# Kernel tuning notes

Measured on AMD Instinct MI355X. Metric: run time of the kernel, lower is better.

Reference implementation:

```python
import jax, jax.numpy as jnp
import numpy as np

QMIN_A, QMAX_A = -128, 127  # int8 activation range
GROUPSIZE = 32


def per_token_quant_dequant(x):
    """Dynamic per-token asymmetric int8 fake-quant (torchao per_token_dynamic_quant)."""
    min_val = jnp.minimum(jnp.min(x, axis=-1, keepdims=True), 0.0)
    max_val = jnp.maximum(jnp.max(x, axis=-1, keepdims=True), 0.0)
    scale = (max_val - min_val) / float(QMAX_A - QMIN_A)
    scale = jnp.maximum(scale, jnp.finfo(x.dtype).eps)
    zp = jnp.clip(QMIN_A - jnp.round(min_val / scale), QMIN_A, QMAX_A)
    q = jnp.clip(jnp.round(x / scale) + zp, QMIN_A, QMAX_A)
    return (q - zp) * scale


def dequant_int4_grouped(w_int, w_scales, w_zeros):
    """w_int: [O, I] int4 values in [-8, 7]; scales/zeros: [O, I//GROUPSIZE]."""
    O, I = w_int.shape
    G = I // GROUPSIZE
    wg = w_int.reshape(O, G, GROUPSIZE).astype(w_scales.dtype)
    w_dq = (wg - w_zeros[:, :, None]) * w_scales[:, :, None]
    return w_dq.reshape(O, I)


def setup_inputs() -> dict:
    key = jax.random.key(0)
    k1, k2, k3 = jax.random.split(key, 3)
    B, S, D_IN, D_OUT = 4, 2048, 2048, 2048
    G = D_IN // GROUPSIZE
    x = jax.random.normal(k1, (B, S, D_IN), dtype=jnp.float32)
    w_int = jax.random.randint(k2, (D_OUT, D_IN), -8, 8, dtype=jnp.int32)
    w_scales = jax.random.uniform(k3, (D_OUT, G), dtype=jnp.float32) * 0.01 + 1e-3
    w_zeros = jnp.zeros((D_OUT, G), dtype=jnp.float32)
    return {"x": x, "w_int": w_int, "w_scales": w_scales, "w_zeros": w_zeros}


def reference(x, w_int, w_scales, w_zeros):
    x_dq = per_token_quant_dequant(x)                  # [B, S, I]
    w_dq = dequant_int4_grouped(w_int, w_scales, w_zeros)  # [O, I]
    return jnp.einsum("bsi,oi->bso", x_dq, w_dq)       # [B, S, O]
```

## Files before the change

kernel.cpp:

```cpp
#include <hip/hip_runtime.h>

#define M_DIM 8192
#define N_DIM 2048
#define K_DIM 2048

#define BM 256
#define BN 256
#define BK 64
#define NT (K_DIM / BK)

#define AS1 __attribute__((address_space(1)))
#define AS3 __attribute__((address_space(3)))

typedef float f32x4 __attribute__((ext_vector_type(4)));
typedef short s16x8 __attribute__((ext_vector_type(8)));

__device__ __forceinline__ unsigned short f2bf(float f) {
  unsigned int u = __float_as_uint(f);
  u += 0x7FFFu + ((u >> 16) & 1u);
  return (unsigned short)(u >> 16);
}

__global__ __launch_bounds__(256) void prep_kernel(
    const float* __restrict__ x, const int* __restrict__ w,
    const float* __restrict__ ws, const float* __restrict__ wz,
    unsigned short* __restrict__ A, unsigned short* __restrict__ W) {
  const int tid = threadIdx.x;
  if (blockIdx.x < M_DIM) {
    const int t = blockIdx.x;
    const float4* r4 = (const float4*)(x + (size_t)t * K_DIM);
    float4 v0 = r4[tid];
    float4 v1 = r4[tid + 256];

    float mn = fminf(fminf(fminf(v0.x, v0.y), fminf(v0.z, v0.w)),
                     fminf(fminf(v1.x, v1.y), fminf(v1.z, v1.w)));
    float mx = fmaxf(fmaxf(fmaxf(v0.x, v0.y), fmaxf(v0.z, v0.w)),
                     fmaxf(fmaxf(v1.x, v1.y), fmaxf(v1.z, v1.w)));
#pragma unroll
    for (int off = 32; off > 0; off >>= 1) {
      mn = fminf(mn, __shfl_xor(mn, off));
      mx = fmaxf(mx, __shfl_xor(mx, off));
    }
    __shared__ float smn[4], smx[4];
    if ((tid & 63) == 0) { smn[tid >> 6] = mn; smx[tid >> 6] = mx; }
    __syncthreads();
    mn = fminf(fminf(smn[0], smn[1]), fminf(smn[2], smn[3]));
    mx = fmaxf(fmaxf(smx[0], smx[1]), fmaxf(smx[2], smx[3]));
    mn = fminf(mn, 0.0f);
    mx = fmaxf(mx, 0.0f);

    float scale = (mx - mn) / 255.0f;
    scale = fmaxf(scale, 1.1920928955078125e-07f);
    const float inv = 1.0f / scale;
    float zp = -128.0f - rintf(mn * inv);
    zp = fminf(fmaxf(zp, -128.0f), 127.0f);

    ushort4* Ao = (ushort4*)(A + (size_t)t * K_DIM);
    {
      float q; ushort4 r;
      q = rintf(v0.x * inv) + zp; q = fminf(fmaxf(q, -128.f), 127.f); r.x = f2bf((q - zp) * scale);
      q = rintf(v0.y * inv) + zp; q = fminf(fmaxf(q, -128.f), 127.f); r.y = f2bf((q - zp) * scale);
      q = rintf(v0.z * inv) + zp; q = fminf(fmaxf(q, -128.f), 127.f); r.z = f2bf((q - zp) * scale);
      q = rintf(v0.w * inv) + zp; q = fminf(fmaxf(q, -128.f), 127.f); r.w = f2bf((q - zp) * scale);
      Ao[tid] = r;
    }
    {
      float q; ushort4 r;
      q = rintf(v1.x * inv) + zp; q = fminf(fmaxf(q, -128.f), 127.f); r.x = f2bf((q - zp) * scale);
      q = rintf(v1.y * inv) + zp; q = fminf(fmaxf(q, -128.f), 127.f); r.y = f2bf((q - zp) * scale);
      q = rintf(v1.z * inv) + zp; q = fminf(fmaxf(q, -128.f), 127.f); r.z = f2bf((q - zp) * scale);
      q = rintf(v1.w * inv) + zp; q = fminf(fmaxf(q, -128.f), 127.f); r.w = f2bf((q - zp) * scale);
      Ao[tid + 256] = r;
    }
  } else {
    const int idx = (blockIdx.x - M_DIM) * 256 + tid;
    const int o  = idx >> 8;
    const int ii = (idx & 255) * 8;
    const int g  = ii >> 5;
    const float s = ws[o * 64 + g];
    const float z = wz[o * 64 + g];
    const int4* wp = (const int4*)(w + (size_t)o * K_DIM + ii);
    int4 a = wp[0], b = wp[1];
    ushort4 r0, r1;
    r0.x = f2bf(((float)a.x - z) * s);
    r0.y = f2bf(((float)a.y - z) * s);
    r0.z = f2bf(((float)a.z - z) * s);
    r0.w = f2bf(((float)a.w - z) * s);
    r1.x = f2bf(((float)b.x - z) * s);
    r1.y = f2bf(((float)b.y - z) * s);
    r1.z = f2bf(((float)b.z - z) * s);
    r1.w = f2bf(((float)b.w - z) * s);
    ushort4* Wo = (ushort4*)(W + (size_t)o * K_DIM + ii);
    Wo[0] = r0;
    Wo[1] = r1;
  }
}


#define SFENCE() __builtin_amdgcn_sched_barrier(0)

#define DSR(dst, addr, IMM)                                                  \
  asm volatile("ds_read_b128 %0, %1 offset:%2"                               \
               : "=v"(dst) : "v"(addr), "i"(IMM))

#define LGKM_GATE(N)                                                         \
  do {                                                                       \
    asm volatile("s_waitcnt lgkmcnt(%0)" :: "i"(N) : "memory");              \
    SFENCE();                                                                \
  } while (0)

#define RD_A(dst, MH, PLIT)                                                  \
  do {                                                                       \
    _Pragma("unroll") for (int i = 0; i < 4; ++i) {                          \
      _Pragma("unroll") for (int kk = 0; kk < 2; ++kk) {                     \
        DSR(dst[i][kk], a_addr[kk],                                          \
            (PLIT) * 32768 + ((MH) * 4 + i) * 2048);                         \
      }                                                                      \
    }                                                                        \
  } while (0)

#define RD_B(dst, NH, PLIT)                                                  \
  do {                                                                       \
    _Pragma("unroll") for (int j = 0; j < 2; ++j) {                          \
      _Pragma("unroll") for (int kk = 0; kk < 2; ++kk) {                     \
        DSR(dst[j][kk], b_addr[kk],                                          \
            (PLIT) * 32768 + ((NH) * 2 + j) * 2048);                         \
      }                                                                      \
    }                                                                        \
  } while (0)

#define MFMA_Q(afX, bfX, MH, NH)                                             \
  do {                                                                       \
    __builtin_amdgcn_s_setprio(1);                                           \
    _Pragma("unroll") for (int kk = 0; kk < 2; ++kk) {                       \
      _Pragma("unroll") for (int i = 0; i < 4; ++i) {                        \
        _Pragma("unroll") for (int j = 0; j < 2; ++j) {                      \
          acc[(MH) * 4 + i][(NH) * 2 + j] =                                  \
              __builtin_amdgcn_mfma_f32_16x16x32_bf16(                       \
                  afX[i][kk], bfX[j][kk],                                    \
                  acc[(MH) * 4 + i][(NH) * 2 + j], 0, 0, 0);                 \
        }                                                                    \
      }                                                                      \
    }                                                                        \
    __builtin_amdgcn_s_setprio(0);                                           \
  } while (0)

#define STAGE_A_HALF(KN, DSTP, H)                                            \
  do {                                                                       \
    _Pragma("unroll") for (int j = 0; j < 2; ++j) {                          \
      __builtin_amdgcn_global_load_lds(                                      \
          (const AS1 void*)(ag + (size_t)((H) * 2 + j) * 64 * K_DIM + (KN)), \
          (AS3 void*)(&As[(DSTP) * (BM * BK) + ((H) * 2 + j) * 4096 + tid * 8]), \
          16, 0, 0);                                                         \
    }                                                                        \
  } while (0)

#define STAGE_B_HALF(KN, DSTP, H)                                            \
  do {                                                                       \
    _Pragma("unroll") for (int j = 0; j < 2; ++j) {                          \
      __builtin_amdgcn_global_load_lds(                                      \
          (const AS1 void*)(bg + (size_t)((H) * 2 + j) * 64 * K_DIM + (KN)), \
          (AS3 void*)(&Bs[(DSTP) * (BN * BK) + ((H) * 2 + j) * 4096 + tid * 8]), \
          16, 0, 0);                                                         \
    }                                                                        \
  } while (0)

#define ITER(KT, PLIT, BN0, BN1)                                             \
  {                                                                          \
    const int k1 = ((KT) + 1) * BK;                                          \
    const int k2 = ((KT) + 2) * BK;                                          \
       \
    RD_B(BN1, 1, PLIT);                                                      \
    RD_A(af1, 1, PLIT);                                                      \
    if ((KT) + 1 < NT) {                                                     \
      STAGE_A_HALF(k1, (PLIT) ^ 1, 1);                                       \
      STAGE_B_HALF(k1, (PLIT) ^ 1, 0);                                       \
      STAGE_B_HALF(k1, (PLIT) ^ 1, 1);                                       \
    }                                                                        \
    SFENCE();                                                                \
    LGKM_GATE(12);                \
    MFMA_Q(af0, BN0, 0, 0);                                                  \
    SFENCE();                                                                \
    LGKM_GATE(8);                                             \
    MFMA_Q(af0, BN1, 0, 1);                                                  \
    SFENCE();                                                                \
    LGKM_GATE(0);                      \
    MFMA_Q(af1, BN1, 1, 1);                                                  \
    SFENCE();                                                                \
    __builtin_amdgcn_s_barrier();             \
    SFENCE();                                                                \
                                                         \
    if ((KT) + 2 < NT) STAGE_A_HALF(k2, PLIT, 0);                            \
    SFENCE();                                                                \
    if ((KT) + 2 < NT) {                                                     \
      asm volatile("s_waitcnt vmcnt(2)" ::: "memory");                       \
    } else {                                                                 \
      asm volatile("s_waitcnt vmcnt(0)" ::: "memory");                       \
    }                                                                        \
    SFENCE();                                                                \
    __builtin_amdgcn_s_barrier();            \
    SFENCE();                                                                \
          \
    if ((KT) + 1 < NT) {                                                     \
      RD_A(af0, 0, (PLIT) ^ 1);                                              \
      RD_B(BN1, 0, (PLIT) ^ 1);          \
    }                                                                        \
    SFENCE();                                                                \
    MFMA_Q(af1, BN0, 1, 0);              \
  }

__global__ __launch_bounds__(512, 2) void gemm_kernel(
    const unsigned short* __restrict__ A,
    const unsigned short* __restrict__ B,
    float* __restrict__ C) {
  __shared__ unsigned short As[2 * BM * BK];
  __shared__ unsigned short Bs[2 * BN * BK];

  const int tid = threadIdx.x;
  const int id  = blockIdx.y * 8 + blockIdx.x;
  const int nid = (id & 7) * 32 + (id >> 3);
  const int bm  = (nid >> 3) * BM;
  const int bn  = (nid & 7) * BN;

  const int lane  = tid & 63;
  const int wv    = tid >> 6;
  const int waveM = (wv >> 2) * 128;
  const int waveN = (wv & 3) * 64;
  const int quad  = lane >> 4;
  const int l16   = lane & 15;

  const int trow = tid >> 3;
  const int phys = (tid & 7) ^ (trow & 7);
  const unsigned short* ag = A + (size_t)(bm + trow) * K_DIM + phys * 8;
  const unsigned short* bg = B + (size_t)(bn + trow) * K_DIM + phys * 8;

  const unsigned asb = (unsigned)(size_t)(AS3 void*)&As[0];
  const unsigned bsb = (unsigned)(size_t)(AS3 void*)&Bs[0];
  unsigned a_addr[2], b_addr[2];
#pragma unroll
  for (int kk = 0; kk < 2; ++kk) {
    const unsigned sw = (unsigned)((quad ^ (l16 & 7) ^ (kk * 4)) * 16);
    a_addr[kk] = asb + (unsigned)((waveM + l16) * BK * 2) + sw;
    b_addr[kk] = bsb + (unsigned)((waveN + l16) * BK * 2) + sw;
  }

  f32x4 acc[8][4] = {};
  s16x8 af0[4][2], af1[4][2];
  s16x8 bX[2][2], bY[2][2];

  STAGE_A_HALF(0, 0, 0);
  STAGE_A_HALF(0, 0, 1);
  STAGE_B_HALF(0, 0, 0);
  STAGE_B_HALF(0, 0, 1);
  STAGE_A_HALF(BK, 1, 0);
  SFENCE();
  asm volatile("s_waitcnt vmcnt(2)" ::: "memory");
  SFENCE();
  __builtin_amdgcn_s_barrier();
  SFENCE();
  RD_A(af0, 0, 0);
  RD_B(bX, 0, 0);
  SFENCE();

  for (int kt = 0; kt < NT; kt += 2) {
    ITER(kt, 0, bX, bY);
    ITER(kt + 1, 1, bY, bX);
  }

#pragma unroll
  for (int mi = 0; mi < 8; ++mi) {
#pragma unroll
    for (int ni = 0; ni < 4; ++ni) {
      const int o = bn + waveN + ni * 16 + l16;
#pragma unroll
      for (int r = 0; r < 4; ++r) {
        const int row = bm + waveM + mi * 16 + quad * 4 + r;
        C[(size_t)row * N_DIM + o] = acc[mi][ni][r];
      }
    }
  }
}

extern "C" void kernel_launch(void* const* d_in, const int* in_sizes, int n_in,
                              void* d_out, int out_size, void* d_ws, size_t ws_size,
                              hipStream_t stream) {
  const float* x        = (const float*)d_in[0];
  const int*   w_int    = (const int*)d_in[1];
  const float* w_scales = (const float*)d_in[2];
  const float* w_zeros  = (const float*)d_in[3];
  float* out = (float*)d_out;

  unsigned short* Aq = (unsigned short*)d_ws;
  unsigned short* Wq = Aq + (size_t)M_DIM * K_DIM;

  const int prep_blocks = M_DIM + (N_DIM * (K_DIM / 8)) / 256;
  prep_kernel<<<prep_blocks, 256, 0, stream>>>(x, w_int, w_scales, w_zeros, Aq, Wq);
  dim3 grid(N_DIM / BN, M_DIM / BM);
  gemm_kernel<<<grid, 512, 0, stream>>>(Aq, Wq, out);
}
```

Baseline: 182.3 us.

## Restructure GEMM main loop into barrier-separated phases with staggered A/B prefetch

Reorganizes each K-iteration of the bf16 MFMA GEMM into four barrier-delimited phases. Each phase reads a fragment from LDS, issues one half-tile global-to-LDS load (A for the next tile, B two tiles ahead), then runs one quadrant of MFMAs. The prologue now preloads B for the first two tiles, and the vmcnt waits are adjusted to match. The aim is to spread LDS reads and global loads evenly across the MFMA work and shorten register lifetimes. The cost is extra workgroup barriers per iteration, which can stall waves.

```diff
diff --git a/kernel.cpp b/kernel.cpp
--- a/kernel.cpp
+++ b/kernel.cpp
@@ -165,48 +165,52 @@
     }                                                                        \
   } while (0)
 
-#define ITER(KT, PLIT, BN0, BN1)                                             \
+#define PHASE_BAR()                                                          \
+  do {                                                                       \
+    SFENCE();                                                                \
+    __builtin_amdgcn_s_barrier();                                            \
+    SFENCE();                                                                \
+  } while (0)
+
+#define ITER(KT, PLIT)                                                       \
   {                                                                          \
     const int k1 = ((KT) + 1) * BK;                                          \
     const int k2 = ((KT) + 2) * BK;                                          \
-       \
-    RD_B(BN1, 1, PLIT);                                                      \
+                    \
+    RD_A(af0, 0, PLIT);                                                      \
+    RD_B(bf0, 0, PLIT);                                                      \
+    if ((KT) + 1 < NT) STAGE_A_HALF(k1, (PLIT) ^ 1, 0);                      \
+    SFENCE();                                                                \
+    LGKM_GATE(8);                \
+    PHASE_BAR();                                                             \
+    LGKM_GATE(0);                                                            \
+    MFMA_Q(af0, bf0, 0, 0);                                                  \
+    PHASE_BAR();                                                             \
+                        \
+    RD_B(bf1, 1, PLIT);                                                      \
+    if ((KT) + 1 < NT) STAGE_A_HALF(k1, (PLIT) ^ 1, 1);                      \
+    PHASE_BAR();                                                             \
+    LGKM_GATE(0);                  \
+    MFMA_Q(af0, bf1, 0, 1);                                                  \
+    PHASE_BAR();                                                             \
+          \
     RD_A(af1, 1, PLIT);                                                      \
-    if ((KT) + 1 < NT) {                                                     \
-      STAGE_A_HALF(k1, (PLIT) ^ 1, 1);                                       \
-      STAGE_B_HALF(k1, (PLIT) ^ 1, 0);                                       \
-      STAGE_B_HALF(k1, (PLIT) ^ 1, 1);                                       \
-    }                                                                        \
-    SFENCE();                                                                \
-    LGKM_GATE(12);                \
-    MFMA_Q(af0, BN0, 0, 0);                                                  \
-    SFENCE();                                                                \
-    LGKM_GATE(8);                                             \
-    MFMA_Q(af0, BN1, 0, 1);                                                  \
-    SFENCE();                                                                \
-    LGKM_GATE(0);                      \
-    MFMA_Q(af1, BN1, 1, 1);                                                  \
-    SFENCE();                                                                \
-    __builtin_amdgcn_s_barrier();             \
-    SFENCE();                                                                \
-                                                         \
-    if ((KT) + 2 < NT) STAGE_A_HALF(k2, PLIT, 0);                            \
-    SFENCE();                                                                \
-    if ((KT) + 2 < NT) {                                                     \
-      asm volatile("s_waitcnt vmcnt(2)" ::: "memory");                       \
+    if ((KT) + 2 < NT) STAGE_B_HALF(k2, PLIT, 0);                            \
+    PHASE_BAR();                                                             \
+    LGKM_GATE(0);                  \
+    MFMA_Q(af1, bf1, 1, 1);                                                  \
+    PHASE_BAR();                                                             \
+          \
+    if ((KT) + 2 < NT) STAGE_B_HALF(k2, PLIT, 1);                            \
+    SFENCE();                                                                \
+    MFMA_Q(af1, bf0, 1, 0);                    \
+    SFENCE();                                                                \
+    if ((KT) < NT - 2) {                                                     \
+      asm volatile("s_waitcnt vmcnt(4)" ::: "memory");                       \
     } else {                                                                 \
       asm volatile("s_waitcnt vmcnt(0)" ::: "memory");                       \
     }                                                                        \
-    SFENCE();                                                                \
-    __builtin_amdgcn_s_barrier();            \
-    SFENCE();                                                                \
-          \
-    if ((KT) + 1 < NT) {                                                     \
-      RD_A(af0, 0, (PLIT) ^ 1);                                              \
-      RD_B(BN1, 0, (PLIT) ^ 1);          \
-    }                                                                        \
-    SFENCE();                                                                \
-    MFMA_Q(af1, BN0, 1, 0);              \
+    PHASE_BAR();                      \
   }
 
 __global__ __launch_bounds__(512, 2) void gemm_kernel(
@@ -246,25 +250,21 @@
 
   f32x4 acc[8][4] = {};
   s16x8 af0[4][2], af1[4][2];
-  s16x8 bX[2][2], bY[2][2];
+  s16x8 bf0[2][2], bf1[2][2];
 
   STAGE_A_HALF(0, 0, 0);
   STAGE_A_HALF(0, 0, 1);
   STAGE_B_HALF(0, 0, 0);
   STAGE_B_HALF(0, 0, 1);
-  STAGE_A_HALF(BK, 1, 0);
+  STAGE_B_HALF(BK, 1, 0);
+  STAGE_B_HALF(BK, 1, 1);
   SFENCE();
-  asm volatile("s_waitcnt vmcnt(2)" ::: "memory");
-  SFENCE();
-  __builtin_amdgcn_s_barrier();
-  SFENCE();
-  RD_A(af0, 0, 0);
-  RD_B(bX, 0, 0);
-  SFENCE();
+  asm volatile("s_waitcnt vmcnt(4)" ::: "memory");
+  PHASE_BAR();
 
   for (int kt = 0; kt < NT; kt += 2) {
-    ITER(kt, 0, bX, bY);
-    ITER(kt + 1, 1, bY, bX);
+    ITER(kt, 0);
+    ITER(kt + 1, 1);
   }
 
 #pragma unroll
```

Measured after the change: 186.3 us. +2.2%, slower.

## Load B fragments directly from global to registers, bypassing LDS staging

Applied to the files above, without the earlier changes.

B tiles are no longer staged through shared memory. Each wave loads its B MFMA fragments straight into registers with global_load_dwordx4, and only A goes through LDS via global_load_lds. The main loop is rescheduled with vmcnt gates and barriers to interleave these register loads with the MFMA quarters. This halves LDS use and removes the B ds_reads, but every wave in the block now fetches B on its own with uncoalesced row-strided accesses, and the pipeline has to hide global latency inside a single iteration.

```diff
diff --git a/kernel.cpp b/kernel.cpp
--- a/kernel.cpp
+++ b/kernel.cpp
@@ -103,9 +103,19 @@
   asm volatile("ds_read_b128 %0, %1 offset:%2"                               \
                : "=v"(dst) : "v"(addr), "i"(IMM))
 
+#define GLB(dst, ptr, IMM)                                                   \
+  asm volatile("global_load_dwordx4 %0, %1, off offset:%2"                   \
+               : "=v"(dst) : "v"(ptr), "i"(IMM))
+
 #define LGKM_GATE(N)                                                         \
   do {                                                                       \
     asm volatile("s_waitcnt lgkmcnt(%0)" :: "i"(N) : "memory");              \
+    SFENCE();                                                                \
+  } while (0)
+
+#define VM_GATE(N)                                                           \
+  do {                                                                       \
+    asm volatile("s_waitcnt vmcnt(%0)" :: "i"(N) : "memory");                \
     SFENCE();                                                                \
   } while (0)
 
@@ -119,13 +129,11 @@
     }                                                                        \
   } while (0)
 
-#define RD_B(dst, NH, PLIT)                                                  \
-  do {                                                                       \
-    _Pragma("unroll") for (int j = 0; j < 2; ++j) {                          \
-      _Pragma("unroll") for (int kk = 0; kk < 2; ++kk) {                     \
-        DSR(dst[j][kk], b_addr[kk],                                          \
-            (PLIT) * 32768 + ((NH) * 2 + j) * 2048);                         \
-      }                                                                      \
+#define RD_A_K(dst, MH, KK, PLIT)                                            \
+  do {                                                                       \
+    _Pragma("unroll") for (int i = 0; i < 4; ++i) {                          \
+      DSR(dst[i][KK], a_addr[KK],                                            \
+          (PLIT) * 32768 + ((MH) * 4 + i) * 2048);                           \
     }                                                                        \
   } while (0)
 
@@ -145,68 +153,52 @@
     __builtin_amdgcn_s_setprio(0);                                           \
   } while (0)
 
-#define STAGE_A_HALF(KN, DSTP, H)                                            \
-  do {                                                                       \
-    _Pragma("unroll") for (int j = 0; j < 2; ++j) {                          \
-      __builtin_amdgcn_global_load_lds(                                      \
-          (const AS1 void*)(ag + (size_t)((H) * 2 + j) * 64 * K_DIM + (KN)), \
-          (AS3 void*)(&As[(DSTP) * (BM * BK) + ((H) * 2 + j) * 4096 + tid * 8]), \
-          16, 0, 0);                                                         \
-    }                                                                        \
-  } while (0)
-
-#define STAGE_B_HALF(KN, DSTP, H)                                            \
-  do {                                                                       \
-    _Pragma("unroll") for (int j = 0; j < 2; ++j) {                          \
-      __builtin_amdgcn_global_load_lds(                                      \
-          (const AS1 void*)(bg + (size_t)((H) * 2 + j) * 64 * K_DIM + (KN)), \
-          (AS3 void*)(&Bs[(DSTP) * (BN * BK) + ((H) * 2 + j) * 4096 + tid * 8]), \
-          16, 0, 0);                                                         \
-    }                                                                        \
-  } while (0)
-
-#define ITER(KT, PLIT, BN0, BN1)                                             \
+#define STAGE_R(KN, DSTP, R)                                                 \
+  __builtin_amdgcn_global_load_lds(                                          \
+      (const AS1 void*)(ag + (size_t)(R) * 64 * K_DIM + (KN)),               \
+      (AS3 void*)(&As[(DSTP) * (BM * BK) + (R) * 4096 + tid * 8]), 16, 0, 0)
+
+#define ITER(KT, PLIT, BP, BJ)                                               \
   {                                                                          \
     const int k1 = ((KT) + 1) * BK;                                          \
-    const int k2 = ((KT) + 2) * BK;                                          \
-       \
-    RD_B(BN1, 1, PLIT);                                                      \
-    RD_A(af1, 1, PLIT);                                                      \
-    if ((KT) + 1 < NT) {                                                     \
-      STAGE_A_HALF(k1, (PLIT) ^ 1, 1);                                       \
-      STAGE_B_HALF(k1, (PLIT) ^ 1, 0);                                       \
-      STAGE_B_HALF(k1, (PLIT) ^ 1, 1);                                       \
-    }                                                                        \
-    SFENCE();                                                                \
-    LGKM_GATE(12);                \
-    MFMA_Q(af0, BN0, 0, 0);                                                  \
-    SFENCE();                                                                \
-    LGKM_GATE(8);                                             \
-    MFMA_Q(af0, BN1, 0, 1);                                                  \
-    SFENCE();                                                                \
-    LGKM_GATE(0);                      \
-    MFMA_Q(af1, BN1, 1, 1);                                                  \
-    SFENCE();                                                                \
-    __builtin_amdgcn_s_barrier();             \
-    SFENCE();                                                                \
-                                                         \
-    if ((KT) + 2 < NT) STAGE_A_HALF(k2, PLIT, 0);                            \
-    SFENCE();                                                                \
-    if ((KT) + 2 < NT) {                                                     \
-      asm volatile("s_waitcnt vmcnt(2)" ::: "memory");                       \
-    } else {                                                                 \
-      asm volatile("s_waitcnt vmcnt(0)" ::: "memory");                       \
-    }                                                                        \
-    SFENCE();                                                                \
-    __builtin_amdgcn_s_barrier();            \
-    SFENCE();                                                                \
-          \
-    if ((KT) + 1 < NT) {                                                     \
-      RD_A(af0, 0, (PLIT) ^ 1);                                              \
-      RD_B(BN1, 0, (PLIT) ^ 1);          \
-    }                                                                        \
-    SFENCE();                                                                \
-    MFMA_Q(af1, BN0, 1, 0);              \
+    const bool pf = (KT) + 1 < NT;                                           \
+                                                             \
+    GLB(BJ[0][0], bg2, 0);   GLB(BJ[0][1], bg2, 64);              \
+    GLB(BJ[1][0], bg3, 0);   GLB(BJ[1][1], bg3, 64);                         \
+    if (pf) { STAGE_R(k1, (PLIT) ^ 1, 0); STAGE_R(k1, (PLIT) ^ 1, 2); }      \
+    RD_A_K(af1, 1, 0, PLIT);                                 \
+    LGKM_GATE(4);                                             \
+    RD_A_K(af1, 1, 1, PLIT);                                  \
+    SFENCE();                                                                \
+    if (pf) { VM_GATE(6); } else { VM_GATE(4); }            \
+    MFMA_Q(af0, BP, 0, 0);                                          \
+    SFENCE();                                                                \
+    if (pf) { VM_GATE(2); } else { VM_GATE(0); }            \
+    MFMA_Q(af0, BJ, 0, 1);                                          \
+    SFENCE();                                                                \
+    VM_GATE(0);                                 \
+    __builtin_amdgcn_s_barrier();         \
+    SFENCE();                                                                \
+                                                             \
+    LGKM_GATE(0);                                             \
+    if (pf) {                                                                \
+      RD_A(af0, 0, (PLIT) ^ 1);              \
+      STAGE_R(k1, (PLIT) ^ 1, 1); STAGE_R(k1, (PLIT) ^ 1, 3);                \
+    }                                                                        \
+    SFENCE();                                                                \
+    MFMA_Q(af1, BJ, 1, 1);                    \
+    SFENCE();                                                                \
+    if (pf) {                                                                \
+      GLB(BJ[0][0], bg0, 128); GLB(BJ[0][1], bg0, 192);     \
+      GLB(BJ[1][0], bg1, 128); GLB(BJ[1][1], bg1, 192);                      \
+    }                                                                        \
+    SFENCE();                                                                \
+    MFMA_Q(af1, BP, 1, 0);                                          \
+    SFENCE();                                                                \
+    if (pf) { VM_GATE(4); } else { VM_GATE(0); }     \
+    __builtin_amdgcn_s_barrier();         \
+    SFENCE();                                                                \
+    bg0 += 64; bg1 += 64; bg2 += 64; bg3 += 64;      \
   }
 
 __global__ __launch_bounds__(512, 2) void gemm_kernel(
@@ -214,7 +206,6 @@
     const unsigned short* __restrict__ B,
     float* __restrict__ C) {
   __shared__ unsigned short As[2 * BM * BK];
-  __shared__ unsigned short Bs[2 * BN * BK];
 
   const int tid = threadIdx.x;
   const int id  = blockIdx.y * 8 + blockIdx.x;
@@ -232,39 +223,40 @@
   const int trow = tid >> 3;
   const int phys = (tid & 7) ^ (trow & 7);
   const unsigned short* ag = A + (size_t)(bm + trow) * K_DIM + phys * 8;
-  const unsigned short* bg = B + (size_t)(bn + trow) * K_DIM + phys * 8;
+
+  const unsigned short* bg0 = B + (size_t)(bn + waveN +  0 + l16) * K_DIM + quad * 8;
+  const unsigned short* bg1 = B + (size_t)(bn + waveN + 16 + l16) * K_DIM + quad * 8;
+  const unsigned short* bg2 = B + (size_t)(bn + waveN + 32 + l16) * K_DIM + quad * 8;
+  const unsigned short* bg3 = B + (size_t)(bn + waveN + 48 + l16) * K_DIM + quad * 8;
 
   const unsigned asb = (unsigned)(size_t)(AS3 void*)&As[0];
-  const unsigned bsb = (unsigned)(size_t)(AS3 void*)&Bs[0];
-  unsigned a_addr[2], b_addr[2];
+  unsigned a_addr[2];
 #pragma unroll
   for (int kk = 0; kk < 2; ++kk) {
     const unsigned sw = (unsigned)((quad ^ (l16 & 7) ^ (kk * 4)) * 16);
     a_addr[kk] = asb + (unsigned)((waveM + l16) * BK * 2) + sw;
-    b_addr[kk] = bsb + (unsigned)((waveN + l16) * BK * 2) + sw;
   }
 
   f32x4 acc[8][4] = {};
   s16x8 af0[4][2], af1[4][2];
-  s16x8 bX[2][2], bY[2][2];
-
-  STAGE_A_HALF(0, 0, 0);
-  STAGE_A_HALF(0, 0, 1);
-  STAGE_B_HALF(0, 0, 0);
-  STAGE_B_HALF(0, 0, 1);
-  STAGE_A_HALF(BK, 1, 0);
+  s16x8 bU[2][2], bV[2][2];
+
+  STAGE_R(0, 0, 0);
+  STAGE_R(0, 0, 1);
+  STAGE_R(0, 0, 2);
+  STAGE_R(0, 0, 3);
+  GLB(bU[0][0], bg0, 0);  GLB(bU[0][1], bg0, 64);
+  GLB(bU[1][0], bg1, 0);  GLB(bU[1][1], bg1, 64);
   SFENCE();
-  asm volatile("s_waitcnt vmcnt(2)" ::: "memory");
-  SFENCE();
+  VM_GATE(4);
   __builtin_amdgcn_s_barrier();
   SFENCE();
   RD_A(af0, 0, 0);
-  RD_B(bX, 0, 0);
   SFENCE();
 
   for (int kt = 0; kt < NT; kt += 2) {
-    ITER(kt, 0, bX, bY);
-    ITER(kt + 1, 1, bY, bX);
+    ITER(kt, 0, bU, bV);
+    ITER(kt + 1, 1, bV, bU);
   }
 
 #pragma unroll
```

Result: slower. 219.5 us (+20.4%).
